# Optimization experiments

Measured on AMD Instinct MI355X. Metric: run time of the kernel, lower is better.

The kernel has to match this reference:

```python
import jax, jax.numpy as jnp
import numpy as np

B, T, D = 2, 2048, 2048
N_HEADS, N_KV = 16, 4
HD = D // N_HEADS  # 128
ROPE_BASE = 10000.0


def _rope_tables(t, dim, base=ROPE_BASE):
    inv_freq = 1.0 / (base ** (jnp.arange(0, dim, 2, dtype=jnp.float32) / dim))
    freqs = jnp.arange(t, dtype=jnp.float32)[:, None] * inv_freq[None, :]  # (T, dim/2)
    emb = jnp.concatenate([freqs, freqs], axis=-1)  # (T, dim)
    return jnp.cos(emb), jnp.sin(emb)


def _rotate_half(x):
    x1, x2 = jnp.split(x, 2, axis=-1)
    return jnp.concatenate([-x2, x1], axis=-1)


def _apply_rope(x, cos, sin):
    # x: (B, H, T, hd); cos/sin: (T, hd)
    return x * cos[None, None] + _rotate_half(x) * sin[None, None]


def setup_inputs() -> dict:
    key = jax.random.key(0)
    ks = jax.random.split(key, 5)
    s = 0.02
    return {
        "x": jax.random.normal(ks[0], (B, T, D), jnp.float32),
        "wq": jax.random.normal(ks[1], (D, N_HEADS * HD), jnp.float32) * s,
        "wk": jax.random.normal(ks[2], (D, N_KV * HD), jnp.float32) * s,
        "wv": jax.random.normal(ks[3], (D, N_KV * HD), jnp.float32) * s,
        "wo": jax.random.normal(ks[4], (D, D), jnp.float32) * s,
    }


def reference(x, wq, wk, wv, wo):
    b, t, c = x.shape
    n_rep = N_HEADS // N_KV
    scale = 1.0 / np.sqrt(HD)

    q = (x @ wq).reshape(b, t, N_HEADS, HD).transpose(0, 2, 1, 3)  # (B,H,T,hd)
    k = (x @ wk).reshape(b, t, N_KV, HD).transpose(0, 2, 1, 3)     # (B,Hkv,T,hd)
    v = (x @ wv).reshape(b, t, N_KV, HD).transpose(0, 2, 1, 3)

    cos, sin = _rope_tables(t, HD)
    q = _apply_rope(q, cos, sin)
    k = _apply_rope(k, cos, sin)

    # repeat_kv (GQA)
    k = jnp.repeat(k, n_rep, axis=1)  # (B,H,T,hd)
    v = jnp.repeat(v, n_rep, axis=1)

    scores = jnp.einsum("bhqd,bhkd->bhqk", q, k) * scale
    causal = jnp.tril(jnp.ones((t, t), dtype=bool))
    scores = jnp.where(causal[None, None], scores, -jnp.inf)
    attn = jax.nn.softmax(scores, axis=-1)
    out = jnp.einsum("bhqk,bhkd->bhqd", attn, v)
    out = out.transpose(0, 2, 1, 3).reshape(b, t, c)
    return out @ wo
```

## Files before the change

kernel.cpp:

```cpp
#include <hip/hip_runtime.h>
#include <hip/hip_bf16.h>
#include <math.h>

#define B_   2
#define T_   2048
#define D_   2048
#define NH_  16
#define NKV_ 4
#define HD_  128
#define MROWS (B_*T_)
#define NQKV  (NH_*HD_ + 2*NKV_*HD_)

typedef __bf16 bf16_t;
typedef __bf16 bf16x8 __attribute__((ext_vector_type(8)));
typedef __bf16 bf16x4 __attribute__((ext_vector_type(4)));
typedef float  floatx4 __attribute__((ext_vector_type(4)));

template <int N> struct IC { static constexpr int v = N; };

__device__ __forceinline__ void async_copy16(const bf16_t* gsrc, bf16_t* ldst) {
  __builtin_amdgcn_global_load_lds(
      (const __attribute__((address_space(1))) unsigned int*)gsrc,
      (__attribute__((address_space(3))) unsigned int*)ldst, 16, 0, 0);
}

__global__ void prep_fused(const float* __restrict__ s0, const float* __restrict__ s1,
                           const float* __restrict__ s2, const float* __restrict__ s3,
                           const float* __restrict__ sx,
                           bf16_t* __restrict__ d0, bf16_t* __restrict__ d1,
                           bf16_t* __restrict__ d2, bf16_t* __restrict__ d3,
                           bf16_t* __restrict__ dx) {
  const int z = blockIdx.z;
  const int tx = threadIdx.x, ty = threadIdx.y;
  if (z == 4) {
    int i = ((blockIdx.y * 64 + blockIdx.x) * 256 + ty * 32 + tx) * 8;
    float4 a = *(const float4*)(sx + i);
    float4 b = *(const float4*)(sx + i + 4);
    bf16x8 v;
    v[0]=(bf16_t)a.x; v[1]=(bf16_t)a.y; v[2]=(bf16_t)a.z; v[3]=(bf16_t)a.w;
    v[4]=(bf16_t)b.x; v[5]=(bf16_t)b.y; v[6]=(bf16_t)b.z; v[7]=(bf16_t)b.w;
    *(bf16x8*)(dx + i) = v;
    return;
  }
  const int N = (z == 1 || z == 2) ? 512 : 2048;
  const int n0 = blockIdx.x * 32;
  if (n0 >= N) return;
  const float* src = (z == 0) ? s0 : (z == 1) ? s1 : (z == 2) ? s2 : s3;
  bf16_t*      dst = (z == 0) ? d0 : (z == 1) ? d1 : (z == 2) ? d2 : d3;
  const int K = 2048;
  __shared__ float tile[32][33];
  int k0 = blockIdx.y * 32;
#pragma unroll
  for (int r = 0; r < 4; r++)
    tile[ty + r*8][tx] = src[(size_t)(k0 + ty + r*8) * N + n0 + tx];
  __syncthreads();
#pragma unroll
  for (int r = 0; r < 4; r++)
    dst[(size_t)(n0 + ty + r*8) * K + k0 + tx] = (bf16_t)tile[tx][ty + r*8];
}

template <typename OUT_T>
__global__ __launch_bounds__(256, 3)
void gemm_bt(const bf16_t* __restrict__ A, const bf16_t* __restrict__ Bt,
             OUT_T* __restrict__ C, int M, int N, int K) {
  __shared__ __align__(16) bf16_t As[128 * 64];
  __shared__ __align__(16) bf16_t Bs[128 * 64];
  const int tid  = threadIdx.x;
  const int wave = tid >> 6, lane = tid & 63;
  const int quad = lane >> 4, l16 = lane & 15;
  const int nBlocksM = M >> 7;
  const int bm = blockIdx.x % nBlocksM, bn = blockIdx.x / nBlocksM;
  const int m0 = bm * 128, n0 = bn * 128;
  const int wm = (wave >> 1) * 64, wn = (wave & 1) * 64;

  floatx4 acc[4][4];
#pragma unroll
  for (int i = 0; i < 4; i++)
#pragma unroll
    for (int j = 0; j < 4; j++) acc[i][j] = floatx4{0.f, 0.f, 0.f, 0.f};

  for (int k0 = 0; k0 < K; k0 += 64) {
    __syncthreads();
#pragma unroll
    for (int i = 0; i < 4; i++) {
      int e = i * 256 + tid;
      int row = e >> 3, grp = e & 7;
      int gg = grp ^ (row & 7);
      async_copy16(A + (size_t)(m0 + row) * K + k0 + gg * 8, As + e * 8);
    }
#pragma unroll
    for (int i = 0; i < 4; i++) {
      int e = i * 256 + tid;
      int row = e >> 3, grp = e & 7;
      int gg = grp ^ (row & 7);
      async_copy16(Bt + (size_t)(n0 + row) * K + k0 + gg * 8, Bs + e * 8);
    }
    __syncthreads();
#pragma unroll
    for (int ks = 0; ks < 2; ks++) {
      bf16x8 af[4], bfr[4];
      int grp = ks * 4 + quad;
#pragma unroll
      for (int mi = 0; mi < 4; mi++) {
        int row = wm + mi * 16 + l16;
        af[mi] = *(const bf16x8*)(As + row * 64 + ((grp ^ (row & 7)) << 3));
      }
#pragma unroll
      for (int ni = 0; ni < 4; ni++) {
        int row = wn + ni * 16 + l16;
        bfr[ni] = *(const bf16x8*)(Bs + row * 64 + ((grp ^ (row & 7)) << 3));
      }
#pragma unroll
      for (int mi = 0; mi < 4; mi++)
#pragma unroll
        for (int ni = 0; ni < 4; ni++)
          acc[mi][ni] = __builtin_amdgcn_mfma_f32_16x16x32_bf16(af[mi], bfr[ni], acc[mi][ni], 0, 0, 0);
    }
  }
#pragma unroll
  for (int mi = 0; mi < 4; mi++) {
#pragma unroll
    for (int r = 0; r < 4; r++) {
      int row = m0 + wm + mi * 16 + quad * 4 + r;
      size_t base = (size_t)row * N + n0 + wn;
#pragma unroll
      for (int ni = 0; ni < 4; ni++)
        C[base + ni * 16 + l16] = (OUT_T)acc[mi][ni][r];
    }
  }
}

#define ROPE_BLOCKS ((MROWS * NKV_ * 64) / 256)
__global__ void kv_prep(const bf16_t* __restrict__ qkv, bf16_t* __restrict__ Kb,
                        bf16_t* __restrict__ Vt) {
  if (blockIdx.x < ROPE_BLOCKS) {
    int g = blockIdx.x * 256 + threadIdx.x;
    int j = g & 63;
    int rest = g >> 6;
    int kvh = rest & 3;
    int row = rest >> 2;
    int t = row & (T_ - 1);
    int b = row >> 11;
    const bf16_t* src = qkv + (size_t)row * NQKV + NH_ * HD_ + kvh * HD_;
    float ang = (float)t * __expf(-0.14391156816f * (float)j);
    float sn, cs;
    __sincosf(ang, &sn, &cs);
    float x0 = (float)src[j];
    float x1 = (float)src[j + 64];
    bf16_t* dst = Kb + ((size_t)(b * NKV_ + kvh) * T_ + t) * HD_;
    dst[j]      = (bf16_t)(x0 * cs - x1 * sn);
    dst[j + 64] = (bf16_t)(x1 * cs + x0 * sn);
    return;
  }
  __shared__ float tile[32][33];
  int bb = blockIdx.x - ROPE_BLOCKS;
  int bx = bb & 63, by = (bb >> 6) & 3, bz = bb >> 8;
  int t0 = bx * 32, d0 = by * 32;
  int b = bz / NKV_, kvh = bz % NKV_;
  int tx = threadIdx.x & 31, ty = threadIdx.x >> 5;
#pragma unroll
  for (int r = 0; r < 4; r++) {
    int t = t0 + ty + r * 8;
    tile[ty + r*8][tx] =
        (float)qkv[(size_t)(b * T_ + t) * NQKV + (NH_ + NKV_) * HD_ + kvh * HD_ + d0 + tx];
  }
  __syncthreads();
#pragma unroll
  for (int r = 0; r < 4; r++) {
    int d = d0 + ty + r * 8;
    int t = t0 + tx;
    int k = t & 63;
    int pos = ((((k >> 4) & 1) * 4 + ((k >> 2) & 3)) << 3) + ((k >> 5) << 2) + (k & 3);
    Vt[((size_t)(b * NKV_ + kvh) * HD_ + d) * T_ + (t & ~63) + pos] =
        (bf16_t)tile[tx][ty + r*8];
  }
}

__global__ __launch_bounds__(256, 2)
void flash_attn(const bf16_t* __restrict__ qkv, const bf16_t* __restrict__ Kb,
                const bf16_t* __restrict__ Vt, bf16_t* __restrict__ Ob) {
  __shared__ __align__(16) bf16_t Ks[2][64 * 128];
  __shared__ __align__(16) bf16_t Vs[2][128 * 64];

  const int tid = threadIdx.x;
  const int wave = tid >> 6, lane = tid & 63;
  const int quad = lane >> 4, l16 = lane & 15;
  const int bid = blockIdx.x;
  const int bh = bid & 31;
  const int jA = bid >> 5;
  const int qtB = 31 - jA;
  const int h = bh & 15;
  const int b = bh >> 4;
  const int kv = h >> 2;
  const int ktB = qtB;

  const bf16_t* kbase = Kb + ((size_t)(b * NKV_ + kv) * T_) * HD_;
  const bf16_t* vbase = Vt + ((size_t)(b * NKV_ + kv) * HD_) * T_;

  auto stage = [&](int kt, int bufi) {
#pragma unroll
    for (int i = 0; i < 4; i++) {
      int e = i * 256 + tid;
      int row = e >> 4, grp = e & 15;
      int gg = grp ^ (row & 15);
      async_copy16(kbase + (size_t)(kt * 64 + row) * HD_ + gg * 8, &Ks[bufi][e * 8]);
    }
#pragma unroll
    for (int i = 0; i < 4; i++) {
      int e = i * 256 + tid;
      int row = e >> 3, grp = e & 7;
      int gg = grp ^ (row & 7);
      async_copy16(vbase + (size_t)row * T_ + kt * 64 + gg * 8, &Vs[bufi][e * 8]);
    }
  };

  stage(0, 0);

  const int qt_g[2] = { qtB, jA };

  bf16x8 qf[2][4];
#pragma unroll
  for (int g = 0; g < 2; g++) {
    const int t_row = qt_g[g] * 64 + wave * 16 + l16;
    const bf16_t* qptr = qkv + (size_t)(b * T_ + t_row) * NQKV + h * HD_;
    bf16x8 qraw[4];
#pragma unroll
    for (int ks = 0; ks < 4; ks++)
      qraw[ks] = *(const bf16x8*)(qptr + ks * 32 + quad * 8);
    const float scale = 0.12751651541057752f;
#pragma unroll
    for (int ks = 0; ks < 2; ks++)
#pragma unroll
      for (int j = 0; j < 8; j++) {
        int d = ks * 32 + quad * 8 + j;
        float ang = (float)t_row * __expf(-0.14391156816f * (float)d);
        float sn, cs;
        __sincosf(ang, &sn, &cs);
        float lo = (float)qraw[ks][j], hi = (float)qraw[ks + 2][j];
        qf[g][ks][j]     = (bf16_t)((lo * cs - hi * sn) * scale);
        qf[g][ks + 2][j] = (bf16_t)((hi * cs + lo * sn) * scale);
      }
  }

  floatx4 o[2][8];
#pragma unroll
  for (int g = 0; g < 2; g++)
#pragma unroll
    for (int i = 0; i < 8; i++) o[g][i] = floatx4{0.f, 0.f, 0.f, 0.f};
  float m_s[2] = {-1e30f, -1e30f}, l_s[2] = {0.f, 0.f};

  const int qlocal64 = wave * 16 + l16;

  for (int kt = 0; kt <= ktB; kt++) {
    const int bufi = kt & 1;
    __syncthreads();
    if (kt < ktB) stage(kt + 1, bufi ^ 1);

    auto body = [&](auto ngc) {
      constexpr int NG = decltype(ngc)::v;
      floatx4 s[NG][4];
#pragma unroll
      for (int g = 0; g < NG; g++)
#pragma unroll
        for (int nt = 0; nt < 4; nt++) s[g][nt] = floatx4{0.f, 0.f, 0.f, 0.f};
      __builtin_amdgcn_s_setprio(1);
#pragma unroll
      for (int ks = 0; ks < 4; ks++) {
        int grp = ks * 4 + quad;
#pragma unroll
        for (int nt = 0; nt < 4; nt++) {
          int row = nt * 16 + l16;
          bf16x8 kf = *(const bf16x8*)(&Ks[bufi][row * 128 + ((grp ^ (row & 15)) << 3)]);
#pragma unroll
          for (int g = 0; g < NG; g++)
            s[g][nt] = __builtin_amdgcn_mfma_f32_16x16x32_bf16(kf, qf[g][ks], s[g][nt], 0, 0, 0);
        }
      }
      __builtin_amdgcn_s_setprio(0);

#pragma unroll
      for (int g = 0; g < NG; g++) {
        if (kt == qt_g[g]) {
#pragma unroll
          for (int nt = 0; nt < 4; nt++)
#pragma unroll
            for (int r = 0; r < 4; r++) {
              int klocal = nt * 16 + quad * 4 + r;
              if (klocal > qlocal64) s[g][nt][r] = -1e30f;
            }
        }
      }

#pragma unroll
      for (int g = 0; g < NG; g++) {
        float mx = fmaxf(fmaxf(s[g][0][0], s[g][0][1]), fmaxf(s[g][0][2], s[g][0][3]));
#pragma unroll
        for (int nt = 1; nt < 4; nt++)
          mx = fmaxf(mx, fmaxf(fmaxf(s[g][nt][0], s[g][nt][1]),
                               fmaxf(s[g][nt][2], s[g][nt][3])));
        mx = fmaxf(mx, __shfl_xor(mx, 16, 64));
        mx = fmaxf(mx, __shfl_xor(mx, 32, 64));
        if (!__all(mx <= m_s[g] + 8.0f)) {
          float mnew = fmaxf(m_s[g], mx);
          float alpha = __builtin_amdgcn_exp2f(m_s[g] - mnew);
          m_s[g] = mnew;
          l_s[g] *= alpha;
#pragma unroll
          for (int dt = 0; dt < 8; dt++) o[g][dt] *= alpha;
        }
        float sum = 0.f;
#pragma unroll
        for (int nt = 0; nt < 4; nt++)
#pragma unroll
          for (int r = 0; r < 4; r++) {
            float p = __builtin_amdgcn_exp2f(s[g][nt][r] - m_s[g]);
            s[g][nt][r] = p;
            sum += p;
          }
        sum += __shfl_xor(sum, 16, 64);
        sum += __shfl_xor(sum, 32, 64);
        l_s[g] += sum;
      }

      __builtin_amdgcn_s_setprio(1);
#pragma unroll
      for (int ks = 0; ks < 2; ks++) {
        bf16x8 pf[NG];
#pragma unroll
        for (int g = 0; g < NG; g++)
#pragma unroll
          for (int j = 0; j < 4; j++) {
            pf[g][j]     = (bf16_t)s[g][ks][j];
            pf[g][j + 4] = (bf16_t)s[g][ks + 2][j];
          }
        const int G = ks * 4 + quad;
#pragma unroll
        for (int dt = 0; dt < 8; dt++) {
          int row = dt * 16 + l16;
          bf16x8 vf = *(const bf16x8*)(&Vs[bufi][row * 64 + ((G ^ (row & 7)) << 3)]);
#pragma unroll
          for (int g = 0; g < NG; g++)
            o[g][dt] = __builtin_amdgcn_mfma_f32_16x16x32_bf16(vf, pf[g], o[g][dt], 0, 0, 0);
        }
      }
      __builtin_amdgcn_s_setprio(0);
    };

    if (kt <= jA) body(IC<2>{});
    else          body(IC<1>{});

  }

#pragma unroll
  for (int g = 0; g < 2; g++) {
    int qg = qt_g[g] * 64 + wave * 16 + l16;
    float inv_l = 1.f / l_s[g];
    size_t base = ((size_t)(b * T_) + qg) * D_ + h * HD_;
#pragma unroll
    for (int dt = 0; dt < 8; dt++) {
      bf16x4 w;
#pragma unroll
      for (int r = 0; r < 4; r++) w[r] = (bf16_t)(o[g][dt][r] * inv_l);
      *(bf16x4*)(Ob + base + dt * 16 + quad * 4) = w;
    }
  }
}

extern "C" void kernel_launch(void* const* d_in, const int* in_sizes, int n_in,
                              void* d_out, int out_size, void* d_ws, size_t ws_size,
                              hipStream_t stream) {
  const float* x  = (const float*)d_in[0];
  const float* wq = (const float*)d_in[1];
  const float* wk = (const float*)d_in[2];
  const float* wv = (const float*)d_in[3];
  const float* wo = (const float*)d_in[4];
  float* out = (float*)d_out;

  bf16_t* x_bf   = (bf16_t*)d_ws;
  bf16_t* attn_o = x_bf;
  bf16_t* wqkv_t = x_bf + (size_t)MROWS * D_;
  bf16_t* wo_t   = wqkv_t + (size_t)NQKV * D_;
  bf16_t* qkv    = wo_t + (size_t)D_ * D_;
  bf16_t* Kb     = qkv + (size_t)MROWS * NQKV;
  bf16_t* Vt     = Kb + (size_t)B_ * NKV_ * T_ * HD_;

  prep_fused<<<dim3(64, 64, 5), dim3(32, 8), 0, stream>>>(
      wq, wk, wv, wo, x,
      wqkv_t, wqkv_t + (size_t)2048 * D_, wqkv_t + (size_t)2560 * D_, wo_t, x_bf);

  gemm_bt<bf16_t><<<(MROWS / 128) * (NQKV / 128), 256, 0, stream>>>(
      x_bf, wqkv_t, qkv, MROWS, NQKV, D_);

  kv_prep<<<ROPE_BLOCKS + (T_ / 32) * (HD_ / 32) * B_ * NKV_, 256, 0, stream>>>(
      qkv, Kb, Vt);

  flash_attn<<<B_ * NH_ * (T_ / 128), 256, 0, stream>>>(qkv, Kb, Vt, attn_o);

  gemm_bt<float><<<(MROWS / 128) * (D_ / 128), 256, 0, stream>>>(
      attn_o, wo_t, out, MROWS, D_, D_);
}
```

Baseline: 280.0 us.

## Pair two 128-row query supertiles per 512-thread attention block sharing KV tiles

The flash attention kernel now launches half as many blocks with 512 threads each. Waves 0-3 handle query supertile j and waves 4-7 handle supertile 15-j, each covering 128 contiguous query rows, so every staged K/V tile in LDS serves eight waves instead of four. The intent is to halve K/V global and LDS staging traffic per query and keep the causal load balanced through the j/15-j pairing. In exchange, waves whose causal range has ended idle at the barriers while the block keeps streaming tiles, and the larger blocks change occupancy and register limits under the new launch bounds.

```diff
diff --git a/kernel.cpp b/kernel.cpp
--- a/kernel.cpp
+++ b/kernel.cpp
@@ -176,7 +176,7 @@
   }
 }
 
-__global__ __launch_bounds__(256, 2)
+__global__ __launch_bounds__(512, 2)
 void flash_attn(const bf16_t* __restrict__ qkv, const bf16_t* __restrict__ Kb,
                 const bf16_t* __restrict__ Vt, bf16_t* __restrict__ Ob) {
   __shared__ __align__(16) bf16_t Ks[2][64 * 128];
@@ -187,27 +187,28 @@
   const int quad = lane >> 4, l16 = lane & 15;
   const int bid = blockIdx.x;
   const int bh = bid & 31;
-  const int jA = bid >> 5;
-  const int qtB = 31 - jA;
+  const int j  = bid >> 5;
   const int h = bh & 15;
   const int b = bh >> 4;
   const int kv = h >> 2;
-  const int ktB = qtB;
+  const int S = (wave < 4) ? j : (15 - j);
+  const int w4 = wave & 3;
+  const int ktLast = 31 - 2 * j;
 
   const bf16_t* kbase = Kb + ((size_t)(b * NKV_ + kv) * T_) * HD_;
   const bf16_t* vbase = Vt + ((size_t)(b * NKV_ + kv) * HD_) * T_;
 
   auto stage = [&](int kt, int bufi) {
 #pragma unroll
-    for (int i = 0; i < 4; i++) {
-      int e = i * 256 + tid;
+    for (int i = 0; i < 2; i++) {
+      int e = i * 512 + tid;
       int row = e >> 4, grp = e & 15;
       int gg = grp ^ (row & 15);
       async_copy16(kbase + (size_t)(kt * 64 + row) * HD_ + gg * 8, &Ks[bufi][e * 8]);
     }
 #pragma unroll
-    for (int i = 0; i < 4; i++) {
-      int e = i * 256 + tid;
+    for (int i = 0; i < 2; i++) {
+      int e = i * 512 + tid;
       int row = e >> 3, grp = e & 7;
       int gg = grp ^ (row & 7);
       async_copy16(vbase + (size_t)row * T_ + kt * 64 + gg * 8, &Vs[bufi][e * 8]);
@@ -216,12 +217,10 @@
 
   stage(0, 0);
 
-  const int qt_g[2] = { qtB, jA };
-
   bf16x8 qf[2][4];
 #pragma unroll
   for (int g = 0; g < 2; g++) {
-    const int t_row = qt_g[g] * 64 + wave * 16 + l16;
+    const int t_row = S * 128 + g * 64 + w4 * 16 + l16;
     const bf16_t* qptr = qkv + (size_t)(b * T_ + t_row) * NQKV + h * HD_;
     bf16x8 qraw[4];
 #pragma unroll
@@ -231,14 +230,14 @@
 #pragma unroll
     for (int ks = 0; ks < 2; ks++)
 #pragma unroll
-      for (int j = 0; j < 8; j++) {
-        int d = ks * 32 + quad * 8 + j;
+      for (int jj = 0; jj < 8; jj++) {
+        int d = ks * 32 + quad * 8 + jj;
         float ang = (float)t_row * __expf(-0.14391156816f * (float)d);
         float sn, cs;
         __sincosf(ang, &sn, &cs);
-        float lo = (float)qraw[ks][j], hi = (float)qraw[ks + 2][j];
-        qf[g][ks][j]     = (bf16_t)((lo * cs - hi * sn) * scale);
-        qf[g][ks + 2][j] = (bf16_t)((hi * cs + lo * sn) * scale);
+        float lo = (float)qraw[ks][jj], hi = (float)qraw[ks + 2][jj];
+        qf[g][ks][jj]     = (bf16_t)((lo * cs - hi * sn) * scale);
+        qf[g][ks + 2][jj] = (bf16_t)((hi * cs + lo * sn) * scale);
       }
   }
 
@@ -249,20 +248,21 @@
     for (int i = 0; i < 8; i++) o[g][i] = floatx4{0.f, 0.f, 0.f, 0.f};
   float m_s[2] = {-1e30f, -1e30f}, l_s[2] = {0.f, 0.f};
 
-  const int qlocal64 = wave * 16 + l16;
-
-  for (int kt = 0; kt <= ktB; kt++) {
+  const int qlocal = w4 * 16 + l16;
+
+  for (int kt = 0; kt <= ktLast; kt++) {
     const int bufi = kt & 1;
     __syncthreads();
-    if (kt < ktB) stage(kt + 1, bufi ^ 1);
-
-    auto body = [&](auto ngc) {
+    if (kt < ktLast) stage(kt + 1, bufi ^ 1);
+
+    auto body = [&](auto ngc, auto g0c) {
       constexpr int NG = decltype(ngc)::v;
+      constexpr int G0 = decltype(g0c)::v;
       floatx4 s[NG][4];
 #pragma unroll
-      for (int g = 0; g < NG; g++)
-#pragma unroll
-        for (int nt = 0; nt < 4; nt++) s[g][nt] = floatx4{0.f, 0.f, 0.f, 0.f};
+      for (int gi = 0; gi < NG; gi++)
+#pragma unroll
+        for (int nt = 0; nt < 4; nt++) s[gi][nt] = floatx4{0.f, 0.f, 0.f, 0.f};
       __builtin_amdgcn_s_setprio(1);
 #pragma unroll
       for (int ks = 0; ks < 4; ks++) {
@@ -272,54 +272,54 @@
           int row = nt * 16 + l16;
           bf16x8 kf = *(const bf16x8*)(&Ks[bufi][row * 128 + ((grp ^ (row & 15)) << 3)]);
 #pragma unroll
-          for (int g = 0; g < NG; g++)
-            s[g][nt] = __builtin_amdgcn_mfma_f32_16x16x32_bf16(kf, qf[g][ks], s[g][nt], 0, 0, 0);
+          for (int gi = 0; gi < NG; gi++)
+            s[gi][nt] = __builtin_amdgcn_mfma_f32_16x16x32_bf16(kf, qf[G0 + gi][ks], s[gi][nt], 0, 0, 0);
         }
       }
       __builtin_amdgcn_s_setprio(0);
 
 #pragma unroll
-      for (int g = 0; g < NG; g++) {
-        if (kt == qt_g[g]) {
+      for (int gi = 0; gi < NG; gi++) {
+        if (kt == 2 * S + G0 + gi) {
 #pragma unroll
           for (int nt = 0; nt < 4; nt++)
 #pragma unroll
             for (int r = 0; r < 4; r++) {
               int klocal = nt * 16 + quad * 4 + r;
-              if (klocal > qlocal64) s[g][nt][r] = -1e30f;
+              if (klocal > qlocal) s[gi][nt][r] = -1e30f;
             }
         }
       }
 
 #pragma unroll
-      for (int g = 0; g < NG; g++) {
-        float mx = fmaxf(fmaxf(s[g][0][0], s[g][0][1]), fmaxf(s[g][0][2], s[g][0][3]));
+      for (int gi = 0; gi < NG; gi++) {
+        float mx = fmaxf(fmaxf(s[gi][0][0], s[gi][0][1]), fmaxf(s[gi][0][2], s[gi][0][3]));
 #pragma unroll
         for (int nt = 1; nt < 4; nt++)
-          mx = fmaxf(mx, fmaxf(fmaxf(s[g][nt][0], s[g][nt][1]),
-                               fmaxf(s[g][nt][2], s[g][nt][3])));
+          mx = fmaxf(mx, fmaxf(fmaxf(s[gi][nt][0], s[gi][nt][1]),
+                               fmaxf(s[gi][nt][2], s[gi][nt][3])));
         mx = fmaxf(mx, __shfl_xor(mx, 16, 64));
         mx = fmaxf(mx, __shfl_xor(mx, 32, 64));
-        if (!__all(mx <= m_s[g] + 8.0f)) {
-          float mnew = fmaxf(m_s[g], mx);
-          float alpha = __builtin_amdgcn_exp2f(m_s[g] - mnew);
-          m_s[g] = mnew;
-          l_s[g] *= alpha;
-#pragma unroll
-          for (int dt = 0; dt < 8; dt++) o[g][dt] *= alpha;
+        if (!__all(mx <= m_s[G0 + gi] + 8.0f)) {
+          float mnew = fmaxf(m_s[G0 + gi], mx);
+          float alpha = __builtin_amdgcn_exp2f(m_s[G0 + gi] - mnew);
+          m_s[G0 + gi] = mnew;
+          l_s[G0 + gi] *= alpha;
+#pragma unroll
+          for (int dt = 0; dt < 8; dt++) o[G0 + gi][dt] *= alpha;
         }
         float sum = 0.f;
 #pragma unroll
         for (int nt = 0; nt < 4; nt++)
 #pragma unroll
           for (int r = 0; r < 4; r++) {
-            float p = __builtin_amdgcn_exp2f(s[g][nt][r] - m_s[g]);
-            s[g][nt][r] = p;
-            sum += p;
+            float pv = __builtin_amdgcn_exp2f(s[gi][nt][r] - m_s[G0 + gi]);
+            s[gi][nt][r] = pv;
+            sum += pv;
           }
         sum += __shfl_xor(sum, 16, 64);
         sum += __shfl_xor(sum, 32, 64);
-        l_s[g] += sum;
+        l_s[G0 + gi] += sum;
       }
 
       __builtin_amdgcn_s_setprio(1);
@@ -327,11 +327,11 @@
       for (int ks = 0; ks < 2; ks++) {
         bf16x8 pf[NG];
 #pragma unroll
-        for (int g = 0; g < NG; g++)
-#pragma unroll
-          for (int j = 0; j < 4; j++) {
-            pf[g][j]     = (bf16_t)s[g][ks][j];
-            pf[g][j + 4] = (bf16_t)s[g][ks + 2][j];
+        for (int gi = 0; gi < NG; gi++)
+#pragma unroll
+          for (int jj = 0; jj < 4; jj++) {
+            pf[gi][jj]     = (bf16_t)s[gi][ks][jj];
+            pf[gi][jj + 4] = (bf16_t)s[gi][ks + 2][jj];
           }
         const int G = ks * 4 + quad;
 #pragma unroll
@@ -339,21 +339,20 @@
           int row = dt * 16 + l16;
           bf16x8 vf = *(const bf16x8*)(&Vs[bufi][row * 64 + ((G ^ (row & 7)) << 3)]);
 #pragma unroll
-          for (int g = 0; g < NG; g++)
-            o[g][dt] = __builtin_amdgcn_mfma_f32_16x16x32_bf16(vf, pf[g], o[g][dt], 0, 0, 0);
+          for (int gi = 0; gi < NG; gi++)
+            o[G0 + gi][dt] = __builtin_amdgcn_mfma_f32_16x16x32_bf16(vf, pf[gi], o[G0 + gi][dt], 0, 0, 0);
         }
       }
       __builtin_amdgcn_s_setprio(0);
     };
 
-    if (kt <= jA) body(IC<2>{});
-    else          body(IC<1>{});
-
+    if (kt <= 2 * S)          body(IC<2>{}, IC<0>{});
+    else if (kt <= 2 * S + 1) body(IC<1>{}, IC<1>{});
   }
 
 #pragma unroll
   for (int g = 0; g < 2; g++) {
-    int qg = qt_g[g] * 64 + wave * 16 + l16;
+    int qg = S * 128 + g * 64 + w4 * 16 + l16;
     float inv_l = 1.f / l_s[g];
     size_t base = ((size_t)(b * T_) + qg) * D_ + h * HD_;
 #pragma unroll
@@ -394,7 +393,7 @@
   kv_prep<<<ROPE_BLOCKS + (T_ / 32) * (HD_ / 32) * B_ * NKV_, 256, 0, stream>>>(
       qkv, Kb, Vt);
 
-  flash_attn<<<B_ * NH_ * (T_ / 128), 256, 0, stream>>>(qkv, Kb, Vt, attn_o);
+  flash_attn<<<B_ * NH_ * (T_ / 256), 512, 0, stream>>>(qkv, Kb, Vt, attn_o);
 
   gemm_bt<float><<<(MROWS / 128) * (D_ / 128), 256, 0, stream>>>(
       attn_o, wo_t, out, MROWS, D_, D_);
```

After: 277.1 us. No clear change (-1.0%).
